# Kernel optimization log

Measured on AMD Instinct MI355X. Metric: run time of the kernel, lower is better.

Reference implementation:

```python
import jax, jax.numpy as jnp
import numpy as np

BN_EPS = 1e-5


def conv_bn_relu(x, w, b, gamma, beta):
    # Conv2d(stride=2, padding=1) -> BatchNorm2d (training-mode batch stats) -> ReLU
    y = jax.lax.conv_general_dilated(
        x, w, window_strides=(2, 2), padding=((1, 1), (1, 1)),
        dimension_numbers=('NCHW', 'OIHW', 'NCHW')) + b[None, :, None, None]
    mu = y.mean(axis=(0, 2, 3))
    var = y.var(axis=(0, 2, 3))
    y = (y - mu[None, :, None, None]) * jax.lax.rsqrt(var + BN_EPS)[None, :, None, None]
    y = y * gamma[None, :, None, None] + beta[None, :, None, None]
    return jax.nn.relu(y)


def setup_inputs() -> dict:
    key = jax.random.key(0)
    ks = jax.random.split(key, 12)
    N, C, HW_IN = 32, 3, 64
    SD = 24           # stem_dim
    RQ = 128          # rnn_hidden_dim
    MD = 128          # module_dim
    FC = 1024         # classifier hidden
    NA = 2            # num answers
    D_PAIR = (SD + 2) * 2 + RQ  # 180
    s = 0.05
    return {
        'image':   jax.random.normal(ks[0], (N, C, HW_IN, HW_IN), jnp.float32),
        'ques':    jax.random.normal(ks[1], (N, RQ), jnp.float32),
        'conv1_w': jax.random.normal(ks[2], (SD, C, 3, 3), jnp.float32) * s,
        'conv1_b': jnp.zeros((SD,), jnp.float32),
        'bn1_g':   jnp.ones((SD,), jnp.float32),
        'bn1_b':   jnp.zeros((SD,), jnp.float32),
        'conv2_w': jax.random.normal(ks[3], (SD, SD, 3, 3), jnp.float32) * s,
        'conv2_b': jnp.zeros((SD,), jnp.float32),
        'bn2_g':   jnp.ones((SD,), jnp.float32),
        'bn2_b':   jnp.zeros((SD,), jnp.float32),
        'w_rel':   jax.random.normal(ks[4], (D_PAIR, MD), jnp.float32) * s,
        'b_rel':   jnp.zeros((MD,), jnp.float32),
        'w_fc1':   jax.random.normal(ks[5], (MD, FC), jnp.float32) * s,
        'b_fc1':   jnp.zeros((FC,), jnp.float32),
        'w_fc2':   jax.random.normal(ks[6], (FC, NA), jnp.float32) * s,
        'b_fc2':   jnp.zeros((NA,), jnp.float32),
    }


def reference(image, ques, conv1_w, conv1_b, bn1_g, bn1_b,
              conv2_w, conv2_b, bn2_g, bn2_b,
              w_rel, b_rel, w_fc1, b_fc1, w_fc2, b_fc2):
    f = conv_bn_relu(image, conv1_w, conv1_b, bn1_g, bn1_b)
    f = conv_bn_relu(f, conv2_w, conv2_b, bn2_g, bn2_b)
    N, F, H, W = f.shape
    HW = H * W
    flat = f.reshape(N, F, HW).transpose(0, 2, 1)      # (N, HW, F)

    # coordinate grid exactly as in the torch code (stacked over (W, H))
    xs = jnp.linspace(-1.0, 1.0, W)
    ys = jnp.linspace(-1.0, 1.0, H)
    xv = jnp.repeat(xs[:, None], H, axis=1)            # (W, H)
    yv = jnp.repeat(ys[None, :], W, axis=0)            # (W, H)
    coords = jnp.stack([xv, yv], axis=2).reshape(-1, 2)  # (HW, 2)

    fc = jnp.concatenate(
        [flat, jnp.broadcast_to(coords[None], (N, HW, 2))], axis=2)  # (N, HW, F+2)
    D = F + 2

    # relation layer is a single Linear over cat([x_i, x_j, ques]) followed by
    # a sum over ALL (HW)^2 pairs. Because the layer is linear, the pair sum
    # decomposes exactly:
    #   sum_{a,b} (fc[b] Wi + fc[a] Wj + q Wq + b_rel)
    # = HW * (sum_p fc[p]) (Wi + Wj) + HW^2 * (q Wq + b_rel)
    Wi, Wj, Wq = w_rel[:D], w_rel[D:2 * D], w_rel[2 * D:]
    s = fc.sum(axis=1)                                  # (N, D)
    hw = jnp.asarray(HW, fc.dtype)
    relations = hw * (s @ (Wi + Wj)) + (hw * hw) * (ques @ Wq + b_rel)  # (N, 128)

    # ---- classifier: Linear -> ReLU -> Linear ----
    h = jax.nn.relu(relations @ w_fc1 + b_fc1)
    out = h @ w_fc2 + b_fc2                             # (N, num_answers)
    return out
```

## Files before the change

### kernel.cpp

```cpp
#include <hip/hip_runtime.h>
#include <math.h>


#define N_BATCH 32
#define C_OUT 24
#define NBLK 192
#define MAGIC 0x13579BDFu
#define AGENT __HIP_MEMORY_SCOPE_AGENT
#define PITCH 40
#define NROWS 33
#define CHSZ (PITCH * NROWS)

__device__ __forceinline__ float aload(const float* p) {
  return __hip_atomic_load(p, __ATOMIC_RELAXED, AGENT);
}
__device__ __forceinline__ void astore(float* p, float v) {
  __hip_atomic_store(p, v, __ATOMIC_RELAXED, AGENT);
}
__device__ __forceinline__ void waitflag(const unsigned* f) {
  while (__hip_atomic_load(f, __ATOMIC_ACQUIRE, AGENT) != MAGIC)
    __builtin_amdgcn_s_sleep(1);
}

__global__ __launch_bounds__(1024) void fused_kernel(
    const float* __restrict__ img, const float* __restrict__ ques,
    const float* __restrict__ c1w, const float* __restrict__ c1b,
    const float* __restrict__ g1,  const float* __restrict__ bt1,
    const float* __restrict__ c2w, const float* __restrict__ c2b,
    const float* __restrict__ g2,  const float* __restrict__ bt2,
    const float* __restrict__ w_rel, const float* __restrict__ b_rel,
    const float* __restrict__ w_fc1, const float* __restrict__ b_fc1,
    const float* __restrict__ w_fc2, const float* __restrict__ b_fc2,
    float* __restrict__ out,
    unsigned* __restrict__ flags1, unsigned* __restrict__ flags2,
    unsigned* __restrict__ flags3,
    float* __restrict__ p1, float* __restrict__ p2,
    float* __restrict__ ssum) {
  const int t = threadIdx.x;
  const int bid = blockIdx.x;
  const int lane = t & 63, wid = t >> 6;
  const int n = bid & 31;
  const int r = bid >> 5;

  __shared__ unsigned short y1u[24 * CHSZ];
  __shared__ float red[5120];
  __shared__ float s_a[C_OUT], s_b[C_OUT];
  __shared__ float a2[4], b2[4];
  __shared__ float chS[16], chS2[16];
  __shared__ float qpart[1024];
  __shared__ float qfull[128];
  __shared__ float s_s[26];
  __shared__ float s_rel[128];
  __shared__ float s_h[1024];

  float h_local = 0.f;

  if (t < 24 * PITCH) {
    int ch = t / PITCH;
    y1u[ch * CHSZ + (t - ch * PITCH)] = 0;
  }
  if (t < 768)
    y1u[(t >> 5) * CHSZ + ((t & 31) + 1) * PITCH] = 0;

  {
    int oh = t >> 5, ow = t & 31;
    float win[27];
    #pragma unroll
    for (int ci = 0; ci < 3; ci++)
      #pragma unroll
      for (int kh = 0; kh < 3; kh++) {
        int ih = oh * 2 - 1 + kh;
        #pragma unroll
        for (int kw = 0; kw < 3; kw++) {
          int iw = ow * 2 - 1 + kw;
          win[ci * 9 + kh * 3 + kw] =
              (ih >= 0 && iw >= 0) ? img[(n * 3 + ci) * 4096 + ih * 64 + iw] : 0.f;
        }
      }
    #pragma unroll
    for (int co = 0; co < C_OUT; co++) {
      float acc = c1b[co];
      #pragma unroll
      for (int q = 0; q < 27; q++) acc += win[q] * c1w[co * 27 + q];
      unsigned bits = __float_as_uint(acc);
      unsigned rr = (bits + 0x7FFFu + ((bits >> 16) & 1u)) >> 16;
      y1u[co * CHSZ + (oh + 1) * PITCH + (ow + 1)] = (unsigned short)rr;
    }
  }
  __syncthreads();

  if (r == 0) {
    if (t < 768) {
      int ch = t >> 5, l = t & 31;
      float s = 0.f, s2 = 0.f;
      #pragma unroll
      for (int i = 0; i < 32; i++) {
        float x = __uint_as_float(
            (unsigned)y1u[ch * CHSZ + (i + 1) * PITCH + (l + 1)] << 16);
        s += x; s2 += x * x;
      }
      #pragma unroll
      for (int off = 16; off > 0; off >>= 1) {
        s += __shfl_down(s, off, 32);
        s2 += __shfl_down(s2, off, 32);
      }
      if (l == 0) {
        astore(&p1[ch * 32 + n], s);
        astore(&p1[768 + ch * 32 + n], s2);
      }
    }
    __syncthreads();
    if (t == 0)
      __hip_atomic_store(&flags1[n], MAGIC, __ATOMIC_RELEASE, AGENT);
  }

  if (t < 32) waitflag(&flags1[t]);
  __syncthreads();
  if (t < 768) {
    int ch = t >> 5, j = t & 31;
    float s = aload(&p1[ch * 32 + j]);
    float s2 = aload(&p1[768 + ch * 32 + j]);
    #pragma unroll
    for (int off = 16; off > 0; off >>= 1) {
      s += __shfl_down(s, off, 32);
      s2 += __shfl_down(s2, off, 32);
    }
    if (j == 0) {
      float mu = s * (1.f / 32768.f);
      float var = s2 * (1.f / 32768.f) - mu * mu;
      float a = rsqrtf(var + 1e-5f) * g1[ch];
      s_a[ch] = a;
      s_b[ch] = bt1[ch] - mu * a;
    }
  }
  __syncthreads();

  const int px = t & 255;
  const int slot = t >> 8;
  const int co2 = r * 4 + slot;
  float acc2;
  {
    const int o2h = px >> 4, o2w = px & 15;
    float accq[4] = {0.f, 0.f, 0.f, 0.f};
    const int ci0 = slot * 6;
    #pragma unroll
    for (int cc = 0; cc < 6; cc++) {
      const int ci = ci0 + cc;
      const float a1 = s_a[ci], b1 = s_b[ci];
      const unsigned* chp = (const unsigned*)(y1u + ci * CHSZ);
      #pragma unroll
      for (int kh = 0; kh < 3; kh++) {
        const int row = o2h * 2 + kh;
        const unsigned* pr = chp + row * (PITCH / 2);
        unsigned w0 = pr[o2w];
        unsigned w1 = pr[o2w + 1];
        float x0 = __uint_as_float(w0 << 16);
        float x1 = __uint_as_float(w0 & 0xffff0000u);
        float x2 = __uint_as_float(w1 << 16);
        x0 = fmaxf(fmaf(x0, a1, b1), 0.f);
        x1 = fmaxf(fmaf(x1, a1, b1), 0.f);
        x2 = fmaxf(fmaf(x2, a1, b1), 0.f);
        if (row == 0) { x0 = 0.f; x1 = 0.f; x2 = 0.f; }
        if (o2w == 0) x0 = 0.f;
        #pragma unroll
        for (int co = 0; co < 4; co++) {
          const float* wp = c2w + ((r * 4 + co) * C_OUT + ci) * 9 + kh * 3;
          accq[co] = fmaf(x0, wp[0], accq[co]);
          accq[co] = fmaf(x1, wp[1], accq[co]);
          accq[co] = fmaf(x2, wp[2], accq[co]);
        }
      }
    }
    #pragma unroll
    for (int q = 0; q < 4; q++) red[(slot * 256 + px) * 5 + q] = accq[q];
  }
  __syncthreads();
  {
    acc2 = c2b[co2];
    #pragma unroll
    for (int s = 0; s < 4; s++) acc2 += red[(s * 256 + px) * 5 + slot];
  }
  {
    float s = acc2, s2 = acc2 * acc2;
    #pragma unroll
    for (int off = 32; off > 0; off >>= 1) {
      s += __shfl_down(s, off, 64);
      s2 += __shfl_down(s2, off, 64);
    }
    if (lane == 0) { chS[slot * 4 + (wid & 3)] = s; chS2[slot * 4 + (wid & 3)] = s2; }
  }
  __syncthreads();
  if (t < 4) {
    float s = chS[t * 4] + chS[t * 4 + 1] + chS[t * 4 + 2] + chS[t * 4 + 3];
    float s2 = chS2[t * 4] + chS2[t * 4 + 1] + chS2[t * 4 + 2] + chS2[t * 4 + 3];
    astore(&p2[(r * 4 + t) * 32 + n], s);
    astore(&p2[768 + (r * 4 + t) * 32 + n], s2);
  }
  __syncthreads();
  if (t == 0)
    __hip_atomic_store(&flags2[bid], MAGIC, __ATOMIC_RELEASE, AGENT);

  if (r == 0) {
    {
      int m = t & 127, g = t >> 7;
      const float* qv = ques + n * 128;
      float q = 0.f;
      for (int k = g * 16; k < g * 16 + 16; k++)
        q += qv[k] * w_rel[(52 + k) * 128 + m];
      qpart[t] = q;
    }
    __syncthreads();
    if (t < 128) {
      float q = b_rel[t];
      #pragma unroll
      for (int g = 0; g < 8; g++) q += qpart[g * 128 + t];
      qfull[t] = 65536.f * q;
    }
    __syncthreads();
    {
      float hl = b_fc1[t];
      #pragma unroll 8
      for (int m = 0; m < 128; m++) hl += qfull[m] * w_fc1[m * 1024 + t];
      h_local = hl;
    }
  }

  if (t < 32) waitflag(&flags2[r * 32 + t]);
  __syncthreads();
  if (t < 128) {
    int c4 = t >> 5, j = t & 31;
    float s = aload(&p2[(r * 4 + c4) * 32 + j]);
    float s2 = aload(&p2[768 + (r * 4 + c4) * 32 + j]);
    #pragma unroll
    for (int off = 16; off > 0; off >>= 1) {
      s += __shfl_down(s, off, 32);
      s2 += __shfl_down(s2, off, 32);
    }
    if (j == 0) {
      float mu = s * (1.f / 8192.f);
      float var = s2 * (1.f / 8192.f) - mu * mu;
      float a = rsqrtf(var + 1e-5f) * g2[r * 4 + c4];
      a2[c4] = a;
      b2[c4] = bt2[r * 4 + c4] - mu * a;
    }
  }
  __syncthreads();

  {
    float v = acc2 * a2[slot] + b2[slot];
    v = v > 0.f ? v : 0.f;
    #pragma unroll
    for (int off = 32; off > 0; off >>= 1) v += __shfl_down(v, off, 64);
    if (lane == 0) chS[slot * 4 + (wid & 3)] = v;
  }
  __syncthreads();
  if (t < 4)
    astore(&ssum[n * C_OUT + r * 4 + t],
           chS[t * 4] + chS[t * 4 + 1] + chS[t * 4 + 2] + chS[t * 4 + 3]);
  __syncthreads();
  if (t == 0)
    __hip_atomic_store(&flags3[bid], MAGIC, __ATOMIC_RELEASE, AGENT);

  if (r != 0) return;

  if (t >= 1 && t < 6) waitflag(&flags3[t * 32 + n]);
  __syncthreads();
  if (t < C_OUT) s_s[t] = aload(&ssum[n * C_OUT + t]);
  if (t == 24 || t == 25) {
    float cs = 0.f;
    for (int i = 0; i < 16; i++) cs += -1.f + 2.f * (float)i / 15.f;
    s_s[t] = 16.f * cs;
  }
  __syncthreads();
  if (t < 128) {
    float sterm = 0.f;
    #pragma unroll
    for (int d = 0; d < 26; d++)
      sterm += s_s[d] * (w_rel[d * 128 + t] + w_rel[(26 + d) * 128 + t]);
    s_rel[t] = 256.f * sterm;
  }
  __syncthreads();

  {
    float acc = h_local;
    #pragma unroll 8
    for (int m = 0; m < 128; m++) acc += s_rel[m] * w_fc1[m * 1024 + t];
    s_h[t] = acc > 0.f ? acc : 0.f;
  }
  __syncthreads();

  {
    float hv = s_h[t];
    float a0 = hv * w_fc2[2 * t], a1 = hv * w_fc2[2 * t + 1];
    #pragma unroll
    for (int off = 32; off > 0; off >>= 1) {
      a0 += __shfl_down(a0, off, 64);
      a1 += __shfl_down(a1, off, 64);
    }
    if (lane == 0) { chS[wid] = a0; chS2[wid] = a1; }
  }
  __syncthreads();
  if (t == 0) {
    float a0 = 0.f, a1 = 0.f;
    #pragma unroll
    for (int i = 0; i < 16; i++) { a0 += chS[i]; a1 += chS2[i]; }
    out[n * 2 + 0] = a0 + b_fc2[0];
    out[n * 2 + 1] = a1 + b_fc2[1];
  }
}

extern "C" void kernel_launch(void* const* d_in, const int* in_sizes, int n_in,
                              void* d_out, int out_size, void* d_ws, size_t ws_size,
                              hipStream_t stream) {
  const float* image   = (const float*)d_in[0];
  const float* ques    = (const float*)d_in[1];
  const float* conv1_w = (const float*)d_in[2];
  const float* conv1_b = (const float*)d_in[3];
  const float* bn1_g   = (const float*)d_in[4];
  const float* bn1_b   = (const float*)d_in[5];
  const float* conv2_w = (const float*)d_in[6];
  const float* conv2_b = (const float*)d_in[7];
  const float* bn2_g   = (const float*)d_in[8];
  const float* bn2_b   = (const float*)d_in[9];
  const float* w_rel   = (const float*)d_in[10];
  const float* b_rel   = (const float*)d_in[11];
  const float* w_fc1   = (const float*)d_in[12];
  const float* b_fc1   = (const float*)d_in[13];
  const float* w_fc2   = (const float*)d_in[14];
  const float* b_fc2   = (const float*)d_in[15];
  float* out = (float*)d_out;

  unsigned* flags1 = (unsigned*)d_ws;
  unsigned* flags2 = flags1 + 32;
  unsigned* flags3 = flags2 + 192;
  float* p1   = (float*)d_ws + 416;
  float* p2   = p1 + 1536;
  float* ssum = p2 + 1536;

  fused_kernel<<<NBLK, 1024, 0, stream>>>(
      image, ques, conv1_w, conv1_b, bn1_g, bn1_b, conv2_w, conv2_b,
      bn2_g, bn2_b, w_rel, b_rel, w_fc1, b_fc1, w_fc2, b_fc2,
      out, flags1, flags2, flags3, p1, p2, ssum);
}
```

Measured before the change: 130.9 us.

## Merge question and relation terms before fc1, vectorize fc1 with split-K, prefetch weights

The question term and the pair-sum term are now added into a single 128-wide coefficient vector before the fc1 matvec. This replaces two 128x1024 passes over w_fc1 with one pass that reads float4 and splits K across four thread groups, reduced through shared memory. The relation-term reduction over 26 rows is also spread across all 1024 threads, the classifier weights are touched early so they sit in cache, and the flag spin-wait uses a relaxed load instead of acquire. The relaxed wait may weaken ordering with the later atomic loads, and the split-K reduction adds two extra barriers.

```diff
diff --git a/kernel.cpp b/kernel.cpp
--- a/kernel.cpp
+++ b/kernel.cpp
@@ -18,7 +18,7 @@
   __hip_atomic_store(p, v, __ATOMIC_RELAXED, AGENT);
 }
 __device__ __forceinline__ void waitflag(const unsigned* f) {
-  while (__hip_atomic_load(f, __ATOMIC_ACQUIRE, AGENT) != MAGIC)
+  while (__hip_atomic_load(f, __ATOMIC_RELAXED, AGENT) != MAGIC)
     __builtin_amdgcn_s_sleep(1);
 }
 
@@ -50,10 +50,8 @@
   __shared__ float qpart[1024];
   __shared__ float qfull[128];
   __shared__ float s_s[26];
-  __shared__ float s_rel[128];
+  __shared__ float s_coef[128];
   __shared__ float s_h[1024];
-
-  float h_local = 0.f;
 
   if (t < 24 * PITCH) {
     int ch = t / PITCH;
@@ -202,6 +200,15 @@
 
   if (r == 0) {
     {
+      float pf = 0.f;
+      #pragma unroll
+      for (int i = 0; i < 4; i++) pf += w_fc1[(t + i * 1024) * 32];
+      if (t < 208) pf += w_rel[t * 32];
+      if (t < 64)  pf += w_fc2[t * 32];
+      if (t < 32)  pf += b_fc1[t * 32];
+      asm volatile("" :: "v"(pf));
+    }
+    {
       int m = t & 127, g = t >> 7;
       const float* qv = ques + n * 128;
       float q = 0.f;
@@ -216,13 +223,6 @@
       for (int g = 0; g < 8; g++) q += qpart[g * 128 + t];
       qfull[t] = 65536.f * q;
     }
-    __syncthreads();
-    {
-      float hl = b_fc1[t];
-      #pragma unroll 8
-      for (int m = 0; m < 128; m++) hl += qfull[m] * w_fc1[m * 1024 + t];
-      h_local = hl;
-    }
   }
 
   if (t < 32) waitflag(&flags2[r * 32 + t]);
@@ -272,20 +272,48 @@
     s_s[t] = 16.f * cs;
   }
   __syncthreads();
+
+  {
+    int col = t & 127, g = t >> 7;
+    float p = 0.f;
+    #pragma unroll
+    for (int dd = 0; dd < 4; dd++) {
+      int d = g + dd * 8;
+      if (d < 26)
+        p += s_s[d] * (w_rel[d * 128 + col] + w_rel[(26 + d) * 128 + col]);
+    }
+    qpart[t] = p;
+  }
+  __syncthreads();
   if (t < 128) {
     float sterm = 0.f;
     #pragma unroll
-    for (int d = 0; d < 26; d++)
-      sterm += s_s[d] * (w_rel[d * 128 + t] + w_rel[(26 + d) * 128 + t]);
-    s_rel[t] = 256.f * sterm;
-  }
-  __syncthreads();
-
-  {
-    float acc = h_local;
+    for (int g = 0; g < 8; g++) sterm += qpart[g * 128 + t];
+    s_coef[t] = qfull[t] + 256.f * sterm;
+  }
+  __syncthreads();
+
+  {
+    const int cg = t & 255, mg = t >> 8;
+    const float4* wp = (const float4*)(w_fc1) + mg * 32 * 256 + cg;
+    float4 acc = make_float4(0.f, 0.f, 0.f, 0.f);
     #pragma unroll 8
-    for (int m = 0; m < 128; m++) acc += s_rel[m] * w_fc1[m * 1024 + t];
-    s_h[t] = acc > 0.f ? acc : 0.f;
+    for (int k = 0; k < 32; k++) {
+      float c = s_coef[mg * 32 + k];
+      float4 w = wp[k * 256];
+      acc.x += c * w.x; acc.y += c * w.y; acc.z += c * w.z; acc.w += c * w.w;
+    }
+    red[cg * 17 + mg * 4 + 0] = acc.x;
+    red[cg * 17 + mg * 4 + 1] = acc.y;
+    red[cg * 17 + mg * 4 + 2] = acc.z;
+    red[cg * 17 + mg * 4 + 3] = acc.w;
+  }
+  __syncthreads();
+  {
+    float h = b_fc1[t];
+    #pragma unroll
+    for (int mg = 0; mg < 4; mg++) h += red[(t >> 2) * 17 + mg * 4 + (t & 3)];
+    s_h[t] = h > 0.f ? h : 0.f;
   }
   __syncthreads();
 
```

New measurement: 120.7 us. -7.8%, faster.
